# Kernel tuning notes

Measured on AMD Instinct MI355X. Metric: run time of the kernel, lower is better.

## Reference

```python
import jax, jax.numpy as jnp
import numpy as np

N, F_IN, D, H = 4096, 128, 128, 4  # nodes, in_features, n_hidden(out_features), n_heads


def setup_inputs() -> dict:
    key = jax.random.key(0)
    ks = jax.random.split(key, 5)
    h = jax.random.normal(ks[0], (N, F_IN), jnp.float32)
    adj_mat = jax.random.randint(ks[1], (N, N), 0, 2, jnp.int32)
    pos = jax.random.normal(ks[2], (N, 3), jnp.float32)
    # xavier_normal-ish scales
    W = jax.random.normal(ks[3], (F_IN, D * H), jnp.float32) * (2.0 / (F_IN + D * H)) ** 0.5
    a = jax.random.normal(ks[4], (H, 2 * D, 1), jnp.float32) * (2.0 / (2 * D + 1)) ** 0.5
    ln_gamma = jnp.ones((D,), jnp.float32)
    ln_beta = jnp.zeros((D,), jnp.float32)
    return dict(h=h, adj_mat=adj_mat, pos=pos, W=W, a=a, ln_gamma=ln_gamma, ln_beta=ln_beta)


def reference(h, adj_mat, pos, W, a, ln_gamma, ln_beta):
    n = h.shape[0]
    ht = (h @ W).reshape(n, H, D).transpose(1, 0, 2)          # (H, N, D)
    src = ht @ a[:, :D, :]                                    # (H, N, 1)
    tgt = ht @ a[:, D:, :]                                    # (H, N, 1)
    diff = pos[:, None, :] - pos[None, :, :]                  # (N, N, 3) rel_pos
    dist = jnp.sqrt(jnp.sum(diff * diff, axis=-1))            # (N, N) cdist p=2
    e = src + jnp.transpose(tgt, (0, 2, 1)) - dist[None]      # (H, N, N)
    e = jnp.where(e > 0, e, 0.2 * e)                          # LeakyReLU(0.2)
    e = jnp.where(adj_mat[None] > 0, e, jnp.float32(-9e15))   # connectivity mask
    attention = jax.nn.softmax(e, axis=-1)                    # (H, N, N)
    h_prime = attention @ ht                                  # (H, N, D)
    hm = jnp.mean(h_prime, axis=0)                            # (N, D) mean over heads
    mu = jnp.mean(hm, axis=-1, keepdims=True)
    var = jnp.var(hm, axis=-1, keepdims=True)
    hn = (hm - mu) / jnp.sqrt(var + 1e-5) * ln_gamma + ln_beta  # LayerNorm
    h_out = h + hn
    att_mean = jnp.mean(attention, axis=0)                    # (N, N)
    delta = jnp.einsum('ij,ijk->ik', att_mean, diff)          # (N, 3)
    pos_out = pos + delta
    return h_out, pos_out
```

## Files before the change

### kernel.cpp

```cpp
#include <hip/hip_runtime.h>
#include <hip/hip_bf16.h>
#include <math.h>

#define NN 4096
#define HH 4

typedef _Float16 h2 __attribute__((ext_vector_type(2)));
typedef _Float16 h4 __attribute__((ext_vector_type(4)));
typedef _Float16 h8 __attribute__((ext_vector_type(8)));
typedef float f4 __attribute__((ext_vector_type(4)));

__global__ __launch_bounds__(512) void k_htgemm(const float* __restrict__ h,
                                                const float* __restrict__ W,
                                                const float* __restrict__ a,
                                                const float* __restrict__ pos,
                                                _Float16* __restrict__ vfrag,
                                                _Float16* __restrict__ posfrag,
                                                float* __restrict__ src,
                                                float* __restrict__ tgt) {
  __shared__ float hs[16][128];
  __shared__ float red[8][16][2];
  const int jt = blockIdx.x;
  const int i0 = jt * 16;
  const int tid = threadIdx.x;
  for (int idx = tid; idx < 16 * 128; idx += 512)
    hs[idx >> 7][idx & 127] = h[(i0 + (idx >> 7)) * 128 + (idx & 127)];
  __syncthreads();
  const int c = tid;
  float acc[16];
#pragma unroll
  for (int r = 0; r < 16; ++r) acc[r] = 0.f;
  for (int k = 0; k < 128; ++k) {
    const float w = W[k * 512 + c];
#pragma unroll
    for (int r = 0; r < 16; ++r) acc[r] = fmaf(hs[r][k], w, acc[r]);
  }
  const int hc = c >> 7, d = c & 127;
  _Float16* vb = vfrag + ((size_t)(hc * 256 + jt) * 64) * 32 + (d >> 4) * 4;
#pragma unroll
  for (int rg = 0; rg < 4; ++rg) {
    h4 v;
    v.x = (_Float16)acc[rg * 4 + 0];
    v.y = (_Float16)acc[rg * 4 + 1];
    v.z = (_Float16)acc[rg * 4 + 2];
    v.w = (_Float16)acc[rg * 4 + 3];
    *(h4*)(vb + ((d & 15) + 16 * rg) * 32) = v;
  }
  const float av = a[hc * 256 + d];
  const float bvv = a[hc * 256 + 128 + d];
  float sv[16], tv[16];
#pragma unroll
  for (int r = 0; r < 16; ++r) { sv[r] = acc[r] * av; tv[r] = acc[r] * bvv; }
#pragma unroll
  for (int off = 32; off >= 1; off >>= 1) {
#pragma unroll
    for (int r = 0; r < 16; ++r) {
      sv[r] += __shfl_xor(sv[r], off, 64);
      tv[r] += __shfl_xor(tv[r], off, 64);
    }
  }
  const int w = tid >> 6;
  if ((tid & 63) == 0) {
#pragma unroll
    for (int r = 0; r < 16; ++r) { red[w][r][0] = sv[r]; red[w][r][1] = tv[r]; }
  }
  if (tid < 64) {
    const int rg = tid >> 4, n = tid & 15;
    h4 pv;
#pragma unroll
    for (int e = 0; e < 4; ++e) {
      const int j = i0 + rg * 4 + e;
      pv[e] = (_Float16)(n < 3 ? pos[j * 3 + n] : (n == 3 ? 1.f : 0.f));
    }
    *(h4*)(posfrag + (size_t)(jt * 64 + tid) * 4) = pv;
  }
  __syncthreads();
  if (tid < 128) {
    const int h2_ = tid >> 5, k = tid & 31, r = k >> 1, st = k & 1;
    const float vsum = red[h2_ * 2][r][st] + red[h2_ * 2 + 1][r][st];
    (st ? tgt : src)[h2_ * NN + i0 + r] = vsum;
  }
}

#define JROW 1032
#define EPS_OFF 0
#define PACC_OFF 65536
#define SMEM_BYTES 67584

__global__ __launch_bounds__(512, 4) void k_attn(
    const _Float16* __restrict__ vfrag, const _Float16* __restrict__ posfrag,
    const int* __restrict__ adj, const float* __restrict__ pos,
    const float* __restrict__ src, const float* __restrict__ tgt,
    __hip_bfloat16* __restrict__ hp_part, __hip_bfloat16* __restrict__ ppart) {
  __shared__ __attribute__((aligned(16))) unsigned char smem[SMEM_BYTES];
  _Float16* dist16 = (_Float16*)smem;

  const int tid = threadIdx.x;
  const int ib = (int)blockIdx.x >> 2, jhb = (int)blockIdx.x & 3;
  const int i0 = ib * 32;
  const int jb = jhb * 1024;

  {
    const int jl = tid & 63, ig = tid >> 6;
    float pix[4], piy[4], piz[4];
#pragma unroll
    for (int q = 0; q < 4; ++q) {
      const int i = ig * 4 + q;
      pix[q] = pos[(i0 + i) * 3 + 0];
      piy[q] = pos[(i0 + i) * 3 + 1];
      piz[q] = pos[(i0 + i) * 3 + 2];
    }
    for (int cc = 0; cc < 8; ++cc) {
      const int jloc = cc * 128 + jl * 2;
      const int j = jb + jloc;
      const float qx0 = pos[j * 3 + 0], qy0 = pos[j * 3 + 1], qz0 = pos[j * 3 + 2];
      const float qx1 = pos[j * 3 + 3], qy1 = pos[j * 3 + 4], qz1 = pos[j * 3 + 5];
#pragma unroll
      for (int q = 0; q < 4; ++q) {
        const int i = ig * 4 + q;
        const int2 av = *(const int2*)(adj + (size_t)(i0 + i) * NN + j);
        float dx = pix[q] - qx0, dy = piy[q] - qy0, dz = piz[q] - qz0;
        const float d0 = sqrtf(dx * dx + dy * dy + dz * dz);
        dx = pix[q] - qx1; dy = piy[q] - qy1; dz = piz[q] - qz1;
        const float d1 = sqrtf(dx * dx + dy * dy + dz * dz);
        h2 dd;
        dd.x = (_Float16)(av.x > 0 ? d0 : 3e4f);
        dd.y = (_Float16)(av.y > 0 ? d1 : 3e4f);
        *(h2*)(dist16 + i * JROW + jloc) = dd;
      }
    }
  }
  __syncthreads();

  const int w = tid >> 6, lane = tid & 63;
  const int hh = w & 3, kp = w >> 2;
  const int il = lane & 15, kg = lane >> 4;

  float srcv[2];
  srcv[0] = src[hh * NN + i0 + il];
  srcv[1] = src[hh * NN + i0 + 16 + il];

  f4 acc[2][8];
#pragma unroll
  for (int mp = 0; mp < 2; ++mp)
#pragma unroll
    for (int dt = 0; dt < 8; ++dt) acc[mp][dt] = (f4){0.f, 0.f, 0.f, 0.f};
  f4 pacc[2];
  pacc[0] = (f4){0.f, 0.f, 0.f, 0.f};
  pacc[1] = (f4){0.f, 0.f, 0.f, 0.f};

  const int jt0 = (jb >> 4) + kp;
  const _Float16* vbase = vfrag + ((size_t)(hh * 256) * 64 + lane) * 32;
  const _Float16* pbase = posfrag + (size_t)lane * 4;
  const float* tbase = tgt + hh * NN + jb + kp * 16 + kg * 4;

#pragma unroll 2
  for (int t = 0; t < 32; ++t) {
    const int jt = jt0 + 2 * t;
    const int toff = (2 * t + kp) * 16;
    const _Float16* vf = vbase + (size_t)jt * 64 * 32;
    const h8 v01 = *(const h8*)(vf);
    const h8 v23 = *(const h8*)(vf + 8);
    const h8 v45 = *(const h8*)(vf + 16);
    const h8 v67 = *(const h8*)(vf + 24);
    h4 vfj[8];
    vfj[0] = __builtin_shufflevector(v01, v01, 0, 1, 2, 3);
    vfj[1] = __builtin_shufflevector(v01, v01, 4, 5, 6, 7);
    vfj[2] = __builtin_shufflevector(v23, v23, 0, 1, 2, 3);
    vfj[3] = __builtin_shufflevector(v23, v23, 4, 5, 6, 7);
    vfj[4] = __builtin_shufflevector(v45, v45, 0, 1, 2, 3);
    vfj[5] = __builtin_shufflevector(v45, v45, 4, 5, 6, 7);
    vfj[6] = __builtin_shufflevector(v67, v67, 0, 1, 2, 3);
    vfj[7] = __builtin_shufflevector(v67, v67, 4, 5, 6, 7);
    const h4 pf = *(const h4*)(pbase + (size_t)jt * 256);
    const float4 tt = *(const float4*)(tbase + 2 * t * 16);
#pragma unroll
    for (int mp = 0; mp < 2; ++mp) {
      const h4 dd = *(const h4*)(dist16 + (mp * 16 + il) * JROW + toff + kg * 4);
      float e0 = (srcv[mp] + tt.x) - (float)dd.x;
      float e1 = (srcv[mp] + tt.y) - (float)dd.y;
      float e2 = (srcv[mp] + tt.z) - (float)dd.z;
      float e3 = (srcv[mp] + tt.w) - (float)dd.w;
      e0 = fmaxf(e0, 0.2f * e0);
      e1 = fmaxf(e1, 0.2f * e1);
      e2 = fmaxf(e2, 0.2f * e2);
      e3 = fmaxf(e3, 0.2f * e3);
      h4 af;
      af.x = (_Float16)__expf(e0);
      af.y = (_Float16)__expf(e1);
      af.z = (_Float16)__expf(e2);
      af.w = (_Float16)__expf(e3);
#pragma unroll
      for (int dt = 0; dt < 8; ++dt)
        acc[mp][dt] = __builtin_amdgcn_mfma_f32_16x16x16f16(af, vfj[dt], acc[mp][dt], 0, 0, 0);
      pacc[mp] = __builtin_amdgcn_mfma_f32_16x16x16f16(af, pf, pacc[mp], 0, 0, 0);
    }
  }

  __syncthreads();
  float* eps = (float*)(smem + EPS_OFF);
  float* pacc_s = (float*)(smem + PACC_OFF);
  if (kp == 1) {
#pragma unroll
    for (int mp = 0; mp < 2; ++mp)
#pragma unroll
      for (int dt = 0; dt < 8; ++dt)
#pragma unroll
        for (int r = 0; r < 4; ++r)
          eps[(hh * 32 + mp * 16 + kg * 4 + r) * 128 + dt * 16 + il] = acc[mp][dt][r];
    if (il < 4) {
#pragma unroll
      for (int mp = 0; mp < 2; ++mp)
#pragma unroll
        for (int r = 0; r < 4; ++r)
          pacc_s[(hh * 32 + mp * 16 + kg * 4 + r) * 4 + il] = pacc[mp][r];
    }
  }
  __syncthreads();
  if (kp == 0) {
    __hip_bfloat16* hpb =
        hp_part + ((size_t)(jhb * 4 + hh) * NN + i0) * 128;
#pragma unroll
    for (int mp = 0; mp < 2; ++mp)
#pragma unroll
      for (int dt = 0; dt < 8; ++dt)
#pragma unroll
        for (int r = 0; r < 4; ++r) {
          const int ii = mp * 16 + kg * 4 + r;
          const float s = acc[mp][dt][r] + eps[(hh * 32 + ii) * 128 + dt * 16 + il];
          hpb[(size_t)ii * 128 + dt * 16 + il] = __float2bfloat16(s);
        }
    if (il < 4) {
#pragma unroll
      for (int mp = 0; mp < 2; ++mp)
#pragma unroll
        for (int r = 0; r < 4; ++r) {
          const int ii = mp * 16 + kg * 4 + r;
          const float s = pacc[mp][r] + pacc_s[(hh * 32 + ii) * 4 + il];
          ppart[((size_t)(jhb * 4 + hh) * NN + i0 + ii) * 4 + il] = __float2bfloat16(s);
        }
    }
  }
}

__global__ __launch_bounds__(128) void k_finish(
    const __hip_bfloat16* __restrict__ hp_part,
    const __hip_bfloat16* __restrict__ ppart, const float* __restrict__ hin,
    const float* __restrict__ pos, const float* __restrict__ gamma,
    const float* __restrict__ beta, float* __restrict__ hout,
    float* __restrict__ out_pos) {
  __shared__ float red[2][2];
  const int i = blockIdx.x, d = threadIdx.x;
  float Li[4];
  float v = 0.f;
#pragma unroll
  for (int hx = 0; hx < 4; ++hx) {
    float L = 0.f, hv = 0.f;
#pragma unroll
    for (int jh = 0; jh < 4; ++jh) {
      L += __bfloat162float(ppart[((size_t)(jh * 4 + hx) * NN + i) * 4 + 3]);
      hv += __bfloat162float(hp_part[((size_t)(jh * 4 + hx) * NN + i) * 128 + d]);
    }
    Li[hx] = 1.f / L;
    v += hv * Li[hx];
  }
  v *= 0.25f;
  float s = v, sq = v * v;
#pragma unroll
  for (int off = 32; off >= 1; off >>= 1) {
    s += __shfl_xor(s, off, 64);
    sq += __shfl_xor(sq, off, 64);
  }
  const int wv = d >> 6;
  if ((d & 63) == 0) { red[wv][0] = s; red[wv][1] = sq; }
  __syncthreads();
  s = red[0][0] + red[1][0];
  sq = red[0][1] + red[1][1];
  const float mu = s * (1.f / 128.f);
  const float var = sq * (1.f / 128.f) - mu * mu;
  const float hn = (v - mu) * rsqrtf(var + 1e-5f) * gamma[d] + beta[d];
  hout[i * 128 + d] = hin[i * 128 + d] + hn;
  if (d < 3) {
    float sp = 0.f;
#pragma unroll
    for (int hx = 0; hx < 4; ++hx) {
      float pv = 0.f;
#pragma unroll
      for (int jh = 0; jh < 4; ++jh)
        pv += __bfloat162float(ppart[((size_t)(jh * 4 + hx) * NN + i) * 4 + d]);
      sp += pv * Li[hx];
    }
    out_pos[i * 3 + d] = 2.f * pos[i * 3 + d] - 0.25f * sp;
  }
}

extern "C" void kernel_launch(void* const* d_in, const int* in_sizes, int n_in,
                              void* d_out, int out_size, void* d_ws, size_t ws_size,
                              hipStream_t stream) {
  const float* h     = (const float*)d_in[0];
  const int*   adj   = (const int*)d_in[1];
  const float* pos   = (const float*)d_in[2];
  const float* W     = (const float*)d_in[3];
  const float* a     = (const float*)d_in[4];
  const float* gamma = (const float*)d_in[5];
  const float* beta  = (const float*)d_in[6];
  float* out = (float*)d_out;

  unsigned char* ws = (unsigned char*)d_ws;
  _Float16* vfrag   = (_Float16*)ws;
  _Float16* posfrag = (_Float16*)(ws + 4194304);
  float* src        = (float*)(ws + 4194304 + 131072);
  float* tgt        = (float*)(ws + 4194304 + 131072 + 65536);
  __hip_bfloat16* hp_part =
      (__hip_bfloat16*)(ws + 4194304 + 131072 + 131072);
  __hip_bfloat16* ppart =
      (__hip_bfloat16*)(ws + 4194304 + 131072 + 131072 + 16777216);

  k_htgemm<<<NN / 16, 512, 0, stream>>>(h, W, a, pos, vfrag, posfrag, src, tgt);
  k_attn<<<(NN / 32) * 4, 512, 0, stream>>>(vfrag, posfrag, adj, pos, src, tgt,
                                            hp_part, ppart);
  k_finish<<<NN, 128, 0, stream>>>(hp_part, ppart, h, pos, gamma, beta, out,
                                   out + NN * 128);
}
```

Baseline: 88.33 us.

## Shrink attention row tile to 16 and software-prefetch V/pos/tgt fragments

The attention kernel's row tile drops from 32 to 16 rows per block, doubling the grid and halving shared memory. This should raise occupancy and parallelism, at the cost of reading each V fragment twice as often. The j-loop now prefetches the next iteration's V, pos and tgt fragments into registers to overlap global loads with MFMA work. The dist/adjacency prologue uses int4/float4 vectorized loads, and blocks are ordered so consecutive blocks share the same j-half.

```diff
diff --git a/kernel.cpp b/kernel.cpp
--- a/kernel.cpp
+++ b/kernel.cpp
@@ -83,9 +83,7 @@
 }
 
 #define JROW 1032
-#define EPS_OFF 0
-#define PACC_OFF 65536
-#define SMEM_BYTES 67584
+#define SMEM_BYTES 33792
 
 __global__ __launch_bounds__(512, 4) void k_attn(
     const _Float16* __restrict__ vfrag, const _Float16* __restrict__ posfrag,
@@ -96,38 +94,36 @@
   _Float16* dist16 = (_Float16*)smem;
 
   const int tid = threadIdx.x;
-  const int ib = (int)blockIdx.x >> 2, jhb = (int)blockIdx.x & 3;
-  const int i0 = ib * 32;
+  const int bid = (int)blockIdx.x;
+  const int ib = bid & 255, jhb = bid >> 8;
+  const int i0 = ib * 16;
   const int jb = jhb * 1024;
 
   {
-    const int jl = tid & 63, ig = tid >> 6;
-    float pix[4], piy[4], piz[4];
-#pragma unroll
-    for (int q = 0; q < 4; ++q) {
-      const int i = ig * 4 + q;
-      pix[q] = pos[(i0 + i) * 3 + 0];
-      piy[q] = pos[(i0 + i) * 3 + 1];
-      piz[q] = pos[(i0 + i) * 3 + 2];
-    }
+    const int si = tid >> 5;
+    const int jc = (tid & 31) * 4;
+    const float pix = pos[(i0 + si) * 3 + 0];
+    const float piy = pos[(i0 + si) * 3 + 1];
+    const float piz = pos[(i0 + si) * 3 + 2];
+    const int* adjp = adj + (size_t)(i0 + si) * NN + jb + jc;
+    const float* posj = pos + (size_t)(jb + jc) * 3;
+#pragma unroll
     for (int cc = 0; cc < 8; ++cc) {
-      const int jloc = cc * 128 + jl * 2;
-      const int j = jb + jloc;
-      const float qx0 = pos[j * 3 + 0], qy0 = pos[j * 3 + 1], qz0 = pos[j * 3 + 2];
-      const float qx1 = pos[j * 3 + 3], qy1 = pos[j * 3 + 4], qz1 = pos[j * 3 + 5];
-#pragma unroll
-      for (int q = 0; q < 4; ++q) {
-        const int i = ig * 4 + q;
-        const int2 av = *(const int2*)(adj + (size_t)(i0 + i) * NN + j);
-        float dx = pix[q] - qx0, dy = piy[q] - qy0, dz = piz[q] - qz0;
-        const float d0 = sqrtf(dx * dx + dy * dy + dz * dz);
-        dx = pix[q] - qx1; dy = piy[q] - qy1; dz = piz[q] - qz1;
-        const float d1 = sqrtf(dx * dx + dy * dy + dz * dz);
-        h2 dd;
-        dd.x = (_Float16)(av.x > 0 ? d0 : 3e4f);
-        dd.y = (_Float16)(av.y > 0 ? d1 : 3e4f);
-        *(h2*)(dist16 + i * JROW + jloc) = dd;
-      }
+      const int4 av = *(const int4*)(adjp + cc * 128);
+      const float4 p0 = *(const float4*)(posj + cc * 384 + 0);
+      const float4 p1 = *(const float4*)(posj + cc * 384 + 4);
+      const float4 p2 = *(const float4*)(posj + cc * 384 + 8);
+      float dx, dy, dz;
+      h4 dd;
+      dx = pix - p0.x; dy = piy - p0.y; dz = piz - p0.z;
+      dd.x = (_Float16)(av.x > 0 ? sqrtf(dx * dx + dy * dy + dz * dz) : 3e4f);
+      dx = pix - p0.w; dy = piy - p1.x; dz = piz - p1.y;
+      dd.y = (_Float16)(av.y > 0 ? sqrtf(dx * dx + dy * dy + dz * dz) : 3e4f);
+      dx = pix - p1.z; dy = piy - p1.w; dz = piz - p2.x;
+      dd.z = (_Float16)(av.z > 0 ? sqrtf(dx * dx + dy * dy + dz * dz) : 3e4f);
+      dx = pix - p2.y; dy = piy - p2.z; dz = piz - p2.w;
+      dd.w = (_Float16)(av.w > 0 ? sqrtf(dx * dx + dy * dy + dz * dz) : 3e4f);
+      *(h4*)(dist16 + si * JROW + jc + cc * 128) = dd;
     }
   }
   __syncthreads();
@@ -136,33 +132,54 @@
   const int hh = w & 3, kp = w >> 2;
   const int il = lane & 15, kg = lane >> 4;
 
-  float srcv[2];
-  srcv[0] = src[hh * NN + i0 + il];
-  srcv[1] = src[hh * NN + i0 + 16 + il];
-
-  f4 acc[2][8];
-#pragma unroll
-  for (int mp = 0; mp < 2; ++mp)
-#pragma unroll
-    for (int dt = 0; dt < 8; ++dt) acc[mp][dt] = (f4){0.f, 0.f, 0.f, 0.f};
-  f4 pacc[2];
-  pacc[0] = (f4){0.f, 0.f, 0.f, 0.f};
-  pacc[1] = (f4){0.f, 0.f, 0.f, 0.f};
+  const float srcv = src[hh * NN + i0 + il];
+
+  f4 acc[8];
+#pragma unroll
+  for (int dt = 0; dt < 8; ++dt) acc[dt] = (f4){0.f, 0.f, 0.f, 0.f};
+  f4 pacc = (f4){0.f, 0.f, 0.f, 0.f};
 
   const int jt0 = (jb >> 4) + kp;
   const _Float16* vbase = vfrag + ((size_t)(hh * 256) * 64 + lane) * 32;
-  const _Float16* pbase = posfrag + (size_t)lane * 4;
+  const _Float16* pbase = posfrag + (size_t)(jt0 * 64 + lane) * 4;
   const float* tbase = tgt + hh * NN + jb + kp * 16 + kg * 4;
-
-#pragma unroll 2
+  const _Float16* ddbase = dist16 + il * JROW + kp * 16 + kg * 4;
+
+  const _Float16* vf0 = vbase + (size_t)jt0 * 2048;
+  h8 a01 = *(const h8*)(vf0);
+  h8 a23 = *(const h8*)(vf0 + 8);
+  h8 a45 = *(const h8*)(vf0 + 16);
+  h8 a67 = *(const h8*)(vf0 + 24);
+  h4 apf = *(const h4*)(pbase);
+  float4 att = *(const float4*)(tbase);
+
   for (int t = 0; t < 32; ++t) {
-    const int jt = jt0 + 2 * t;
-    const int toff = (2 * t + kp) * 16;
-    const _Float16* vf = vbase + (size_t)jt * 64 * 32;
-    const h8 v01 = *(const h8*)(vf);
-    const h8 v23 = *(const h8*)(vf + 8);
-    const h8 v45 = *(const h8*)(vf + 16);
-    const h8 v67 = *(const h8*)(vf + 24);
+    const h8 v01 = a01, v23 = a23, v45 = a45, v67 = a67;
+    const h4 pf = apf;
+    const float4 tt = att;
+    if (t < 31) {
+      const _Float16* vfn = vbase + (size_t)(jt0 + 2 * (t + 1)) * 2048;
+      a01 = *(const h8*)(vfn);
+      a23 = *(const h8*)(vfn + 8);
+      a45 = *(const h8*)(vfn + 16);
+      a67 = *(const h8*)(vfn + 24);
+      apf = *(const h4*)(pbase + (t + 1) * 512);
+      att = *(const float4*)(tbase + (t + 1) * 32);
+    }
+    const h4 dd = *(const h4*)(ddbase + t * 32);
+    float e0 = (srcv + tt.x) - (float)dd.x;
+    float e1 = (srcv + tt.y) - (float)dd.y;
+    float e2 = (srcv + tt.z) - (float)dd.z;
+    float e3 = (srcv + tt.w) - (float)dd.w;
+    e0 = fmaxf(e0, 0.2f * e0);
+    e1 = fmaxf(e1, 0.2f * e1);
+    e2 = fmaxf(e2, 0.2f * e2);
+    e3 = fmaxf(e3, 0.2f * e3);
+    h4 af;
+    af.x = (_Float16)__expf(e0);
+    af.y = (_Float16)__expf(e1);
+    af.z = (_Float16)__expf(e2);
+    af.w = (_Float16)__expf(e3);
     h4 vfj[8];
     vfj[0] = __builtin_shufflevector(v01, v01, 0, 1, 2, 3);
     vfj[1] = __builtin_shufflevector(v01, v01, 4, 5, 6, 7);
@@ -172,73 +189,45 @@
     vfj[5] = __builtin_shufflevector(v45, v45, 4, 5, 6, 7);
     vfj[6] = __builtin_shufflevector(v67, v67, 0, 1, 2, 3);
     vfj[7] = __builtin_shufflevector(v67, v67, 4, 5, 6, 7);
-    const h4 pf = *(const h4*)(pbase + (size_t)jt * 256);
-    const float4 tt = *(const float4*)(tbase + 2 * t * 16);
-#pragma unroll
-    for (int mp = 0; mp < 2; ++mp) {
-      const h4 dd = *(const h4*)(dist16 + (mp * 16 + il) * JROW + toff + kg * 4);
-      float e0 = (srcv[mp] + tt.x) - (float)dd.x;
-      float e1 = (srcv[mp] + tt.y) - (float)dd.y;
-      float e2 = (srcv[mp] + tt.z) - (float)dd.z;
-      float e3 = (srcv[mp] + tt.w) - (float)dd.w;
-      e0 = fmaxf(e0, 0.2f * e0);
-      e1 = fmaxf(e1, 0.2f * e1);
-      e2 = fmaxf(e2, 0.2f * e2);
-      e3 = fmaxf(e3, 0.2f * e3);
-      h4 af;
-      af.x = (_Float16)__expf(e0);
-      af.y = (_Float16)__expf(e1);
-      af.z = (_Float16)__expf(e2);
-      af.w = (_Float16)__expf(e3);
-#pragma unroll
-      for (int dt = 0; dt < 8; ++dt)
-        acc[mp][dt] = __builtin_amdgcn_mfma_f32_16x16x16f16(af, vfj[dt], acc[mp][dt], 0, 0, 0);
-      pacc[mp] = __builtin_amdgcn_mfma_f32_16x16x16f16(af, pf, pacc[mp], 0, 0, 0);
-    }
-  }
-
-  __syncthreads();
-  float* eps = (float*)(smem + EPS_OFF);
-  float* pacc_s = (float*)(smem + PACC_OFF);
+#pragma unroll
+    for (int dt = 0; dt < 8; ++dt)
+      acc[dt] = __builtin_amdgcn_mfma_f32_16x16x16f16(af, vfj[dt], acc[dt], 0, 0, 0);
+    pacc = __builtin_amdgcn_mfma_f32_16x16x16f16(af, pf, pacc, 0, 0, 0);
+  }
+
+  __syncthreads();
+  float* eps = (float*)smem;
+  float* pacc_s = (float*)(smem + 32768);
   if (kp == 1) {
 #pragma unroll
-    for (int mp = 0; mp < 2; ++mp)
-#pragma unroll
-      for (int dt = 0; dt < 8; ++dt)
-#pragma unroll
-        for (int r = 0; r < 4; ++r)
-          eps[(hh * 32 + mp * 16 + kg * 4 + r) * 128 + dt * 16 + il] = acc[mp][dt][r];
+    for (int dt = 0; dt < 8; ++dt)
+#pragma unroll
+      for (int r = 0; r < 4; ++r)
+        eps[(hh * 16 + kg * 4 + r) * 128 + dt * 16 + il] = acc[dt][r];
     if (il < 4) {
 #pragma unroll
-      for (int mp = 0; mp < 2; ++mp)
-#pragma unroll
-        for (int r = 0; r < 4; ++r)
-          pacc_s[(hh * 32 + mp * 16 + kg * 4 + r) * 4 + il] = pacc[mp][r];
+      for (int r = 0; r < 4; ++r)
+        pacc_s[(hh * 16 + kg * 4 + r) * 4 + il] = pacc[r];
     }
   }
   __syncthreads();
   if (kp == 0) {
-    __hip_bfloat16* hpb =
-        hp_part + ((size_t)(jhb * 4 + hh) * NN + i0) * 128;
-#pragma unroll
-    for (int mp = 0; mp < 2; ++mp)
-#pragma unroll
-      for (int dt = 0; dt < 8; ++dt)
-#pragma unroll
-        for (int r = 0; r < 4; ++r) {
-          const int ii = mp * 16 + kg * 4 + r;
-          const float s = acc[mp][dt][r] + eps[(hh * 32 + ii) * 128 + dt * 16 + il];
-          hpb[(size_t)ii * 128 + dt * 16 + il] = __float2bfloat16(s);
-        }
+    __hip_bfloat16* hpb = hp_part + ((size_t)(jhb * 4 + hh) * NN + i0) * 128;
+#pragma unroll
+    for (int dt = 0; dt < 8; ++dt)
+#pragma unroll
+      for (int r = 0; r < 4; ++r) {
+        const int ii = kg * 4 + r;
+        const float s = acc[dt][r] + eps[(hh * 16 + ii) * 128 + dt * 16 + il];
+        hpb[(size_t)ii * 128 + dt * 16 + il] = __float2bfloat16(s);
+      }
     if (il < 4) {
 #pragma unroll
-      for (int mp = 0; mp < 2; ++mp)
-#pragma unroll
-        for (int r = 0; r < 4; ++r) {
-          const int ii = mp * 16 + kg * 4 + r;
-          const float s = pacc[mp][r] + pacc_s[(hh * 32 + ii) * 4 + il];
-          ppart[((size_t)(jhb * 4 + hh) * NN + i0 + ii) * 4 + il] = __float2bfloat16(s);
-        }
+      for (int r = 0; r < 4; ++r) {
+        const int ii = kg * 4 + r;
+        const float s = pacc[r] + pacc_s[(hh * 16 + ii) * 4 + il];
+        ppart[((size_t)(jhb * 4 + hh) * NN + i0 + ii) * 4 + il] = __float2bfloat16(s);
+      }
     }
   }
 }
@@ -317,7 +306,7 @@
       (__hip_bfloat16*)(ws + 4194304 + 131072 + 131072 + 16777216);
 
   k_htgemm<<<NN / 16, 512, 0, stream>>>(h, W, a, pos, vfrag, posfrag, src, tgt);
-  k_attn<<<(NN / 32) * 4, 512, 0, stream>>>(vfrag, posfrag, adj, pos, src, tgt,
+  k_attn<<<(NN / 16) * 4, 512, 0, stream>>>(vfrag, posfrag, adj, pos, src, tgt,
                                             hp_part, ppart);
   k_finish<<<NN, 128, 0, stream>>>(hp_part, ppart, h, pos, gamma, beta, out,
                                    out + NN * 128);
```

Result: slower. 125.9 us (+42.5%).
